# Optimization experiments

Hardware: AMD Instinct MI355X
Metric: run time of the kernel (lower is better)

The kernel has to match this reference:

```python
import jax, jax.numpy as jnp
import numpy as np

N, E = 50000, 800000
IN_C, H_C, OUT_C, HEADS = 64, 32, 32, 8


def setup_inputs() -> dict:
    key = jax.random.key(0)
    ks = jax.random.split(key, 16)
    def glorot(k, shape):
        fan_in = shape[-1]
        return jax.random.normal(k, shape, dtype=jnp.float32) / jnp.sqrt(jnp.float32(fan_in))
    inp = {
        'x': jax.random.normal(ks[0], (N, IN_C), dtype=jnp.float32),
        'edge_index': jax.random.randint(ks[1], (2, E), 0, N, dtype=jnp.int64),
        # layer 1: in_c -> h_c, heads
        'W1l': glorot(ks[2], (HEADS * H_C, IN_C)),
        'b1l': jnp.zeros((HEADS * H_C,), jnp.float32),
        'W1r': glorot(ks[3], (HEADS * H_C, IN_C)),
        'b1r': jnp.zeros((HEADS * H_C,), jnp.float32),
        'att1': glorot(ks[4], (HEADS, H_C)),
        'bias1': jnp.zeros((H_C,), jnp.float32),
        # layer 2: h_c -> out_c, heads
        'W2l': glorot(ks[5], (HEADS * OUT_C, H_C)),
        'b2l': jnp.zeros((HEADS * OUT_C,), jnp.float32),
        'W2r': glorot(ks[6], (HEADS * OUT_C, H_C)),
        'b2r': jnp.zeros((HEADS * OUT_C,), jnp.float32),
        'att2': glorot(ks[7], (HEADS, OUT_C)),
        'bias2': jnp.zeros((OUT_C,), jnp.float32),
    }
    return inp


def _gatv2_layer(x, src, dst, valid, Wl, bl, Wr, br, att, bias):
    # PyG GATv2Conv (share_weights=False, concat=False): message j->i uses
    # e = att . leaky_relu(lin_l(x_j) + lin_r(x_i), 0.2); softmax over dst; agg lin_l(x_j).
    n = x.shape[0]
    heads, c = att.shape
    xl = (x @ Wl.T + bl).reshape(n, heads, c)
    xr = (x @ Wr.T + br).reshape(n, heads, c)
    m = jax.nn.leaky_relu(xl[src] + xr[dst], negative_slope=0.2)  # [Etot,H,C]
    score = jnp.einsum('ehc,hc->eh', m, att)                      # [Etot,H]
    score = jnp.where(valid[:, None], score, -jnp.inf)
    smax = jax.ops.segment_max(score, dst, num_segments=n)        # [N,H]
    a = jnp.where(valid[:, None], jnp.exp(score - smax[dst]), 0.0)
    denom = jax.ops.segment_sum(a, dst, num_segments=n)
    a = a / jnp.maximum(denom[dst], 1e-16)
    out = jax.ops.segment_sum(a[..., None] * xl[src], dst, num_segments=n)  # [N,H,C]
    return out.mean(axis=1) + bias


def reference(x, edge_index, W1l, b1l, W1r, b1r, att1, bias1,
              W2l, b2l, W2r, b2r, att2, bias2):
    n = x.shape[0]
    src0, dst0 = edge_index[0], edge_index[1]
    # PyG removes existing self loops then adds fresh ones: mask originals,
    # append one self loop per node (keeps static shapes).
    loop = jnp.arange(n, dtype=src0.dtype)
    src = jnp.concatenate([src0, loop])
    dst = jnp.concatenate([dst0, loop])
    valid = jnp.concatenate([src0 != dst0, jnp.ones((n,), bool)])
    h = _gatv2_layer(x, src, dst, valid, W1l, b1l, W1r, b1r, att1, bias1)
    h = jax.nn.leaky_relu(h, negative_slope=0.01)  # nn.LeakyReLU default
    out = _gatv2_layer(h, src, dst, valid, W2l, b2l, W2r, b2r, att2, bias2)
    return out
```

## Files before the change

### kernel.cpp

```cpp
#include <hip/hip_runtime.h>
#include <math.h>

#define HEADS 8
#define CDIM 32
#define ODIM 256
#define BKT_SHIFT 7
#define CHUNK 4096
#define CAP 4096
#define GB 512

typedef _Float16 h2 __attribute__((ext_vector_type(2)));
typedef _Float16 h4 __attribute__((ext_vector_type(4)));
typedef _Float16 h8 __attribute__((ext_vector_type(8)));
typedef float f32x4 __attribute__((ext_vector_type(4)));
typedef unsigned long long u64;
union H4 { h4 v; h2 p[2]; u64 u; };

#if __has_builtin(__builtin_amdgcn_fdot2)
#define FDOT2(a,b,c) __builtin_amdgcn_fdot2((a),(b),(c),false)
#else
static __device__ __forceinline__ float fdot2_sw(h2 a, h2 b, float c){
  return fmaf((float)a.x, (float)b.x, fmaf((float)a.y, (float)b.y, c));
}
#define FDOT2(a,b,c) fdot2_sw((a),(b),(c))
#endif

__device__ __forceinline__ float lrelu(float v, float s){ return fmaxf(v, s*v); }


__global__ __launch_bounds__(512) void csr_offs_kernel(
    int* __restrict__ hist, int* __restrict__ btotal, int NB, int B){
  __shared__ int s[512];
  int b = blockIdx.x, t = threadIdx.x;
  int v = (t < NB) ? hist[t*B + b] : 0;
  s[t] = v;
  __syncthreads();
  for (int off=1; off<512; off<<=1){
    int u = (t >= off) ? s[t-off] : 0;
    __syncthreads(); s[t] += u; __syncthreads();
  }
  int excl = s[t] - v;
  if (t < NB) hist[t*B + b] = excl;
  if (t == NB-1) btotal[b] = excl + v;
}

__global__ __launch_bounds__(512) void csr_scatter_kernel(
    const int* __restrict__ src, const int* __restrict__ dst,
    const int* __restrict__ rank, const int* __restrict__ offs,
    int* __restrict__ bpack, int e, int B){
  int t = threadIdx.x, k = blockIdx.x;
  int base_i = k*CHUNK;
#pragma unroll
  for (int j = 0; j < CHUNK/512; ++j){
    int i = base_i + j*512 + t;
    if (i < e){
      int r = rank[i];
      if (r >= 0){
        int d = dst[i], sv = src[i];
        int b = d >> BKT_SHIFT;
        int pos = b*CAP + offs[k*B + b] + r;
        bpack[pos] = (sv << BKT_SHIFT) | (d & 127);
      }
    }
  }
}

__global__ __launch_bounds__(512) void csr_sort_kernel(
    const int* __restrict__ bpack, const int* __restrict__ btotal,
    int* __restrict__ csr, int* __restrict__ ind_beg, int* __restrict__ ind_end,
    int n, int B){
  __shared__ int lh[128], cur[128], ss[128];
  int b = blockIdx.x, t = threadIdx.x;
  int beg = b*CAP;
  int cnt = btotal[b]; if (cnt > CAP) cnt = CAP;
  if (t < 128) lh[t] = 0;
  __syncthreads();
  for (int j = t; j < cnt; j += 512)
    atomicAdd(&lh[bpack[beg+j] & 127], 1);
  __syncthreads();
  int v = (t < 128) ? lh[t] : 0;
  if (t < 128) ss[t] = v;
  __syncthreads();
  for (int off=1; off<128; off<<=1){
    int u = (t >= off && t < 128) ? ss[t-off] : 0;
    __syncthreads();
    if (t < 128) ss[t] += u;
    __syncthreads();
  }
  if (t < 128){
    int excl = ss[t] - v;
    cur[t] = excl;
    int node = (b << BKT_SHIFT) + t;
    if (node < n){ ind_beg[node] = beg + excl; ind_end[node] = beg + excl + v; }
  }
  __syncthreads();
  for (int j = t; j < cnt; j += 512){
    int p = bpack[beg + j];
    int lpos = atomicAdd(&cur[p & 127], 1);
    csr[beg + lpos] = p >> BKT_SHIFT;
  }
}

template<int K, bool FUSE_AUX, bool W_F32>
__global__ __launch_bounds__(512) void gemm_mfma(const float* __restrict__ X,
    const void* __restrict__ Wl, const float* __restrict__ bl,
    const void* __restrict__ Wr, const float* __restrict__ br,
    _Float16* __restrict__ outl, _Float16* __restrict__ outr, int n,
    const int* __restrict__ src, const int* __restrict__ dst,
    int* __restrict__ rank, int* __restrict__ hist, int e, int B,
    const float* __restrict__ W2l, const float* __restrict__ W2r,
    _Float16* __restrict__ w2lh, _Float16* __restrict__ w2rh){
  if (FUSE_AUX && blockIdx.y == 1){
    int k = blockIdx.x;
    int NB = (e + CHUNK-1)/CHUNK;
    int t = threadIdx.x;
    if (k < NB){
      __shared__ int lh[512];
      lh[t] = 0;
      __syncthreads();
      int base_i = k*CHUNK;
#pragma unroll
      for (int j = 0; j < CHUNK/512; ++j){
        int i = base_i + j*512 + t;
        if (i < e){
          int s = src[i], d = dst[i];
          int r = -1;
          if (s != d) r = atomicAdd(&lh[d>>BKT_SHIFT], 1);
          rank[i] = r;
        }
      }
      __syncthreads();
      for (int b = t; b < B; b += 512) hist[k*B + b] = lh[b];
    } else if (k < NB + 8){
      int i = ((k - NB)*512 + t)*4;
      const float* s; _Float16* d; int off;
      if (i < 8192){ s = W2l; d = w2lh; off = i; }
      else         { s = W2r; d = w2rh; off = i - 8192; }
      float4 v = *(const float4*)(s + off);
      *(h4*)(d + off) = (h4){(_Float16)v.x, (_Float16)v.y, (_Float16)v.z, (_Float16)v.w};
    }
    return;
  }
  const int KP = K + 8;
  const int NKS = K/32;
  const int NLD = (64*(K/4))/512;
  __shared__ __align__(16) _Float16 Xs[2][64*(K+8)];
  int t = threadIdx.x;
  int nt = (n + 63) >> 6;
  int tb0 = blockIdx.x;
  int tb1 = blockIdx.x + GB;
  bool has1 = (tb1 < nt);

#pragma unroll
  for (int j = 0; j < NLD; ++j){
    int idx = t + j*512;
    int row = idx/(K/4), c = (idx%(K/4))*4;
    int node = tb0*64 + row; if (node >= n) node = n-1;
    f32x4 xv = __builtin_nontemporal_load((const f32x4*)(X + (size_t)node*K + c));
    *(h4*)(Xs[0] + row*KP + c) = (h4){(_Float16)xv[0], (_Float16)xv[1],
                                      (_Float16)xv[2], (_Float16)xv[3]};
  }
  f32x4 p1[NLD];
  if (has1){
#pragma unroll
    for (int j = 0; j < NLD; ++j){
      int idx = t + j*512;
      int row = idx/(K/4), c = (idx%(K/4))*4;
      int node = tb1*64 + row; if (node >= n) node = n-1;
      p1[j] = __builtin_nontemporal_load((const f32x4*)(X + (size_t)node*K + c));
    }
  }
  __syncthreads();

  int wave = t >> 6, lane = t & 63;
  int co = wave*64;
  const void* W   = (co < 256) ? Wl : Wr;
  const float* Bv = (co < 256) ? bl : br;
  _Float16* outp  = (co < 256) ? outl : outr;
  int lco = co & 255;
  int lr = lane & 15, lg = lane >> 4;

  h8 wf[NKS][4];
#pragma unroll
  for (int ks = 0; ks < NKS; ++ks){
    int k0 = ks*32 + lg*8;
#pragma unroll
    for (int c = 0; c < 4; ++c){
      if (W_F32){
        const float* wp = (const float*)W + (size_t)(lco + c*16 + lr)*K + k0;
        float4 w0 = *(const float4*)(wp);
        float4 w1 = *(const float4*)(wp + 4);
        wf[ks][c] = (h8){(_Float16)w0.x,(_Float16)w0.y,(_Float16)w0.z,(_Float16)w0.w,
                         (_Float16)w1.x,(_Float16)w1.y,(_Float16)w1.z,(_Float16)w1.w};
      } else {
        wf[ks][c] = *(const h8*)((const _Float16*)W + (size_t)(lco + c*16 + lr)*K + k0);
      }
    }
  }

  float4 bb[4];
#pragma unroll
  for (int c = 0; c < 4; ++c) bb[c] = *(const float4*)(Bv + lco + c*16 + lg*4);

  auto compute = [&](const _Float16* buf, int n0){
    f32x4 acc[4][4];
#pragma unroll
    for (int c = 0; c < 4; ++c)
#pragma unroll
      for (int m = 0; m < 4; ++m) acc[c][m] = (f32x4){0.f, 0.f, 0.f, 0.f};
#pragma unroll
    for (int ks = 0; ks < NKS; ++ks){
      int k0 = ks*32 + lg*8;
      h8 b[4];
#pragma unroll
      for (int m = 0; m < 4; ++m)
        b[m] = *(const h8*)(buf + (m*16 + lr)*KP + k0);
#pragma unroll
      for (int c = 0; c < 4; ++c)
#pragma unroll
        for (int m = 0; m < 4; ++m)
          acc[c][m] = __builtin_amdgcn_mfma_f32_16x16x32_f16(wf[ks][c], b[m], acc[c][m], 0, 0, 0);
    }
#pragma unroll
    for (int c = 0; c < 4; ++c){
      int ch = lco + c*16 + lg*4;
#pragma unroll
      for (int m = 0; m < 4; ++m){
        int node = n0 + m*16 + lr;
        if (node < n){
          h4 o = {(_Float16)(acc[c][m][0] + bb[c].x), (_Float16)(acc[c][m][1] + bb[c].y),
                  (_Float16)(acc[c][m][2] + bb[c].z), (_Float16)(acc[c][m][3] + bb[c].w)};
          *(h4*)(outp + (size_t)node*ODIM + ch) = o;
        }
      }
    }
  };

  compute(Xs[0], tb0*64);

  if (has1){
#pragma unroll
    for (int j = 0; j < NLD; ++j){
      int idx = t + j*512;
      int row = idx/(K/4), c = (idx%(K/4))*4;
      *(h4*)(Xs[1] + row*KP + c) = (h4){(_Float16)p1[j][0], (_Float16)p1[j][1],
                                        (_Float16)p1[j][2], (_Float16)p1[j][3]};
    }
    __syncthreads();
    compute(Xs[1], tb1*64);
  }
}

__global__ __launch_bounds__(256) void edge_kernel(
    const _Float16* __restrict__ xl, const _Float16* __restrict__ xr,
    const float* __restrict__ att, const float* __restrict__ bias,
    const int* __restrict__ ind_beg, const int* __restrict__ ind_end,
    const int* __restrict__ csr_src,
    float* __restrict__ out, int n, int act)
{
  int wid = blockIdx.x*4 + (threadIdx.x >> 6);
  if (wid >= n) return;
  int lane = threadIdx.x & 63;
  const float LOG2E = 1.44269504088896341f;

  float4 attf = *(const float4*)(att + 4*lane);
  h2 at0 = (h2){(_Float16)(attf.x*LOG2E), (_Float16)(attf.y*LOG2E)};
  h2 at1 = (h2){(_Float16)(attf.z*LOG2E), (_Float16)(attf.w*LOG2E)};
  const h2 c02 = {(_Float16)0.2f, (_Float16)0.2f};

  H4 xrh; xrh.u = __builtin_nontemporal_load((const u64*)(xr + (size_t)wid*ODIM + 4*lane));
  H4 self; self.v = *(const h4*)(xl + (size_t)wid*ODIM + 4*lane);

  auto score = [&](const H4& c)->float{
    h2 t0 = c.p[0] + xrh.p[0];
    h2 t1 = c.p[1] + xrh.p[1];
    h2 q0 = __builtin_elementwise_max(t0, t0 * c02);
    h2 q1 = __builtin_elementwise_max(t1, t1 * c02);
    float d = FDOT2(q0, at0, FDOT2(q1, at1, 0.f));
    d += __shfl_xor(d, 1);
    d += __shfl_xor(d, 2);
    d += __shfl_xor(d, 4);
    return d;
  };

  float w0 = exp2f(score(self));
  float denom = w0;
  float4 acc;
  acc.x = w0 * (float)self.v.x;
  acc.y = w0 * (float)self.v.y;
  acc.z = w0 * (float)self.v.z;
  acc.w = w0 * (float)self.v.w;

  int beg = __builtin_amdgcn_readfirstlane(ind_beg[wid]);
  int end = __builtin_amdgcn_readfirstlane(ind_end[wid]);
  int cnt = end - beg;

#define GATHER(j) (*(const h4*)(xl + (size_t)((unsigned)__shfl(sidx,(j)))*ODIM + 4*lane))
  for (int cb = 0; cb < cnt; cb += 64){
    int ccnt = min(cnt - cb, 64);
    int sidx = (lane < ccnt) ? __builtin_nontemporal_load(csr_src + beg + cb + lane) : 0;
    H4 r0, r1, r2, r3;
    r0.v = (h4){}; r1.v = (h4){}; r2.v = (h4){}; r3.v = (h4){};
    if (ccnt > 0) r0.v = GATHER(0);
    if (ccnt > 1) r1.v = GATHER(1);
    if (ccnt > 2) r2.v = GATHER(2);
    if (ccnt > 3) r3.v = GATHER(3);
#pragma unroll 2
    for (int k = 0; k < ccnt; k += 2){
      H4 e0 = r0, e1 = r1;
      r0 = r2; r1 = r3;
      if (k+4 < ccnt) r2.v = GATHER(k+4);
      if (k+5 < ccnt) r3.v = GATHER(k+5);
      float s0 = score(e0);
      float s1 = score(e1);
      float pe0 = exp2f(s0);
      float pe1 = (k+1 < ccnt) ? exp2f(s1) : 0.f;
      denom += pe0 + pe1;
      acc.x = fmaf(pe0, (float)e0.v.x, fmaf(pe1, (float)e1.v.x, acc.x));
      acc.y = fmaf(pe0, (float)e0.v.y, fmaf(pe1, (float)e1.v.y, acc.y));
      acc.z = fmaf(pe0, (float)e0.v.z, fmaf(pe1, (float)e1.v.z, acc.z));
      acc.w = fmaf(pe0, (float)e0.v.w, fmaf(pe1, (float)e1.v.w, acc.w));
    }
  }
#undef GATHER

  float inv = 1.f/denom;
  float vx = acc.x*inv, vy = acc.y*inv, vz = acc.z*inv, vw = acc.w*inv;
  vx += __shfl_xor(vx, 8);  vx += __shfl_xor(vx, 16);  vx += __shfl_xor(vx, 32);
  vy += __shfl_xor(vy, 8);  vy += __shfl_xor(vy, 16);  vy += __shfl_xor(vy, 32);
  vz += __shfl_xor(vz, 8);  vz += __shfl_xor(vz, 16);  vz += __shfl_xor(vz, 32);
  vw += __shfl_xor(vw, 8);  vw += __shfl_xor(vw, 16);  vw += __shfl_xor(vw, 32);
  if (lane < 8){
    float4 bv = *(const float4*)(bias + 4*lane);
    float ox = vx*0.125f + bv.x;
    float oy = vy*0.125f + bv.y;
    float oz = vz*0.125f + bv.z;
    float ow = vw*0.125f + bv.w;
    if (act){
      ox = lrelu(ox, 0.01f); oy = lrelu(oy, 0.01f);
      oz = lrelu(oz, 0.01f); ow = lrelu(ow, 0.01f);
    }
    f32x4 ov = {ox, oy, oz, ow};
    __builtin_nontemporal_store(ov, (f32x4*)(out + (size_t)wid*CDIM + 4*lane));
  }
}

extern "C" void kernel_launch(void* const* d_in, const int* in_sizes, int n_in,
                              void* d_out, int out_size, void* d_ws, size_t ws_size,
                              hipStream_t stream){
  (void)n_in; (void)out_size; (void)ws_size;
  const float* x    = (const float*)d_in[0];
  const int*   ei   = (const int*)d_in[1];
  const float* W1l  = (const float*)d_in[2];
  const float* b1l  = (const float*)d_in[3];
  const float* W1r  = (const float*)d_in[4];
  const float* b1r  = (const float*)d_in[5];
  const float* att1 = (const float*)d_in[6];
  const float* bias1= (const float*)d_in[7];
  const float* W2l  = (const float*)d_in[8];
  const float* b2l  = (const float*)d_in[9];
  const float* W2r  = (const float*)d_in[10];
  const float* b2r  = (const float*)d_in[11];
  const float* att2 = (const float*)d_in[12];
  const float* bias2= (const float*)d_in[13];
  int n = in_sizes[0] / 64;
  int e = in_sizes[1] / 2;
  const int* srcp = ei;
  const int* dstp = ei + e;

  char* ws = (char*)d_ws;
  size_t off = 0;
  auto alloc = [&](size_t bytes)->char*{
    char* p = ws + off; off += (bytes + 255) & ~(size_t)255; return p;
  };
  _Float16* xl  = (_Float16*)alloc((size_t)n*ODIM*2);
  _Float16* xr  = (_Float16*)alloc((size_t)n*ODIM*2);
  float* h      = (float*)alloc((size_t)n*CDIM*4);
  int*   ind_beg = (int*)alloc((size_t)n*4);
  int*   ind_end = (int*)alloc((size_t)n*4);
  int*   rank   = (int*)alloc((size_t)e*4);

  int NB = (e + CHUNK-1) / CHUNK;
  int B  = (n + 127) >> 7;
  int*   csr    = (int*)alloc((size_t)B*CAP*4);
  int*   bpack  = (int*)alloc((size_t)B*CAP*4);
  _Float16* w2lh = (_Float16*)alloc((size_t)ODIM*32*2);
  _Float16* w2rh = (_Float16*)alloc((size_t)ODIM*32*2);
  int*   hist   = (int*)alloc((size_t)NB*B*4);
  int*   btotal = (int*)alloc((size_t)B*4);

  gemm_mfma<64,true,true><<<dim3(GB,2), 512, 0, stream>>>(
      x, W1l, b1l, W1r, b1r, xl, xr, n, srcp, dstp, rank, hist, e, B,
      W2l, W2r, w2lh, w2rh);
  csr_offs_kernel<<<B, 512, 0, stream>>>(hist, btotal, NB, B);
  csr_scatter_kernel<<<NB, 512, 0, stream>>>(srcp, dstp, rank, hist, bpack, e, B);
  csr_sort_kernel<<<B, 512, 0, stream>>>(bpack, btotal, csr, ind_beg, ind_end, n, B);

  edge_kernel<<<(n+3)/4, 256, 0, stream>>>(xl, xr, att1, bias1, ind_beg, ind_end, csr, h, n, 1);
  gemm_mfma<32,false,false><<<dim3(GB,1), 512, 0, stream>>>(
      h, w2lh, b2l, w2rh, b2r, xl, xr, n, nullptr, nullptr, nullptr, nullptr, 0, 0,
      nullptr, nullptr, nullptr, nullptr);
  edge_kernel<<<(n+3)/4, 256, 0, stream>>>(xl, xr, att2, bias2, ind_beg, ind_end, csr, (float*)d_out, n, 0);
}
```

Measured before the change: 288.1 us.

## Fuse CSR bucket offsets and scatter into histogram pass via global atomics

Replaces the separate per-chunk histogram, offset-scan and scatter kernels with a single pass inside the fused aux branch. Each chunk reserves a contiguous range per bucket with one global atomicAdd and scatters packed edges immediately, keeping ranks in registers. This removes two kernel launches and the rank/hist round-trips through global memory, at the cost of a memset and a nondeterministic edge order within buckets, which the later sort kernel still handles per node.

```diff
diff --git a/kernel.cpp b/kernel.cpp
--- a/kernel.cpp
+++ b/kernel.cpp
@@ -27,43 +27,6 @@
 
 __device__ __forceinline__ float lrelu(float v, float s){ return fmaxf(v, s*v); }
 
-
-__global__ __launch_bounds__(512) void csr_offs_kernel(
-    int* __restrict__ hist, int* __restrict__ btotal, int NB, int B){
-  __shared__ int s[512];
-  int b = blockIdx.x, t = threadIdx.x;
-  int v = (t < NB) ? hist[t*B + b] : 0;
-  s[t] = v;
-  __syncthreads();
-  for (int off=1; off<512; off<<=1){
-    int u = (t >= off) ? s[t-off] : 0;
-    __syncthreads(); s[t] += u; __syncthreads();
-  }
-  int excl = s[t] - v;
-  if (t < NB) hist[t*B + b] = excl;
-  if (t == NB-1) btotal[b] = excl + v;
-}
-
-__global__ __launch_bounds__(512) void csr_scatter_kernel(
-    const int* __restrict__ src, const int* __restrict__ dst,
-    const int* __restrict__ rank, const int* __restrict__ offs,
-    int* __restrict__ bpack, int e, int B){
-  int t = threadIdx.x, k = blockIdx.x;
-  int base_i = k*CHUNK;
-#pragma unroll
-  for (int j = 0; j < CHUNK/512; ++j){
-    int i = base_i + j*512 + t;
-    if (i < e){
-      int r = rank[i];
-      if (r >= 0){
-        int d = dst[i], sv = src[i];
-        int b = d >> BKT_SHIFT;
-        int pos = b*CAP + offs[k*B + b] + r;
-        bpack[pos] = (sv << BKT_SHIFT) | (d & 127);
-      }
-    }
-  }
-}
 
 __global__ __launch_bounds__(512) void csr_sort_kernel(
     const int* __restrict__ bpack, const int* __restrict__ btotal,
@@ -107,7 +70,7 @@
     const void* __restrict__ Wr, const float* __restrict__ br,
     _Float16* __restrict__ outl, _Float16* __restrict__ outr, int n,
     const int* __restrict__ src, const int* __restrict__ dst,
-    int* __restrict__ rank, int* __restrict__ hist, int e, int B,
+    int* __restrict__ bpack, int* __restrict__ bucket_cnt, int e, int B,
     const float* __restrict__ W2l, const float* __restrict__ W2r,
     _Float16* __restrict__ w2lh, _Float16* __restrict__ w2rh){
   if (FUSE_AUX && blockIdx.y == 1){
@@ -115,22 +78,32 @@
     int NB = (e + CHUNK-1)/CHUNK;
     int t = threadIdx.x;
     if (k < NB){
-      __shared__ int lh[512];
+      __shared__ int lh[512], bs[512];
       lh[t] = 0;
       __syncthreads();
       int base_i = k*CHUNK;
+      int rr[CHUNK/512], dd[CHUNK/512], sv[CHUNK/512];
 #pragma unroll
       for (int j = 0; j < CHUNK/512; ++j){
         int i = base_i + j*512 + t;
+        rr[j] = -1; dd[j] = 0; sv[j] = 0;
         if (i < e){
           int s = src[i], d = dst[i];
-          int r = -1;
-          if (s != d) r = atomicAdd(&lh[d>>BKT_SHIFT], 1);
-          rank[i] = r;
+          dd[j] = d; sv[j] = s;
+          if (s != d) rr[j] = atomicAdd(&lh[d>>BKT_SHIFT], 1);
         }
       }
       __syncthreads();
-      for (int b = t; b < B; b += 512) hist[k*B + b] = lh[b];
+      for (int b = t; b < B; b += 512)
+        bs[b] = lh[b] ? atomicAdd(bucket_cnt + b, lh[b]) : 0;
+      __syncthreads();
+#pragma unroll
+      for (int j = 0; j < CHUNK/512; ++j){
+        if (rr[j] >= 0){
+          int b = dd[j] >> BKT_SHIFT;
+          bpack[b*CAP + bs[b] + rr[j]] = (sv[j] << BKT_SHIFT) | (dd[j] & 127);
+        }
+      }
     } else if (k < NB + 8){
       int i = ((k - NB)*512 + t)*4;
       const float* s; _Float16* d; int off;
@@ -378,23 +351,20 @@
   float* h      = (float*)alloc((size_t)n*CDIM*4);
   int*   ind_beg = (int*)alloc((size_t)n*4);
   int*   ind_end = (int*)alloc((size_t)n*4);
-  int*   rank   = (int*)alloc((size_t)e*4);
 
   int NB = (e + CHUNK-1) / CHUNK;
   int B  = (n + 127) >> 7;
   int*   csr    = (int*)alloc((size_t)B*CAP*4);
   int*   bpack  = (int*)alloc((size_t)B*CAP*4);
+  int*   bucket_cnt = (int*)alloc((size_t)B*4);
   _Float16* w2lh = (_Float16*)alloc((size_t)ODIM*32*2);
   _Float16* w2rh = (_Float16*)alloc((size_t)ODIM*32*2);
-  int*   hist   = (int*)alloc((size_t)NB*B*4);
-  int*   btotal = (int*)alloc((size_t)B*4);
-
+
+  hipMemsetAsync(bucket_cnt, 0, (size_t)B*4, stream);
   gemm_mfma<64,true,true><<<dim3(GB,2), 512, 0, stream>>>(
-      x, W1l, b1l, W1r, b1r, xl, xr, n, srcp, dstp, rank, hist, e, B,
+      x, W1l, b1l, W1r, b1r, xl, xr, n, srcp, dstp, bpack, bucket_cnt, e, B,
       W2l, W2r, w2lh, w2rh);
-  csr_offs_kernel<<<B, 512, 0, stream>>>(hist, btotal, NB, B);
-  csr_scatter_kernel<<<NB, 512, 0, stream>>>(srcp, dstp, rank, hist, bpack, e, B);
-  csr_sort_kernel<<<B, 512, 0, stream>>>(bpack, btotal, csr, ind_beg, ind_end, n, B);
+  csr_sort_kernel<<<B, 512, 0, stream>>>(bpack, bucket_cnt, csr, ind_beg, ind_end, n, B);
 
   edge_kernel<<<(n+3)/4, 256, 0, stream>>>(xl, xr, att1, bias1, ind_beg, ind_end, csr, h, n, 1);
   gemm_mfma<32,false,false><<<dim3(GB,1), 512, 0, stream>>>(
```

After: 283.4 us. Within noise of the previous version (-1.6%).
